# Optimization experiments

Hardware: AMD Instinct MI355X
Metric: run time of the kernel (lower is better)

## Reference

```python
import jax, jax.numpy as jnp
import numpy as np

SRC, B, SNT, E, C, V, EXT = 512, 16, 512, 512, 512, 12000, 500


def setup_inputs() -> dict:
    key = jax.random.key(0)
    ks = jax.random.split(key, 12)
    alignment_weight = jax.random.uniform(ks[0], (SRC, B, SNT), dtype=jnp.float32)
    arc_weight = jax.random.uniform(ks[1], (SRC, B, SRC), dtype=jnp.float32)
    rel_weight = jnp.zeros((1,), jnp.float32)
    concept_outs = jax.random.normal(ks[2], (SRC, B, E), dtype=jnp.float32)
    copy_seq = jax.random.randint(ks[3], (SNT, B, 2), 0, V + EXT)
    # pin the max so tot_ext = V + EXT is deterministic (torch uses copy_seq.max().item())
    copy_seq = copy_seq.at[0, 0, 0].set(V + EXT - 1)
    target = jax.random.randint(ks[4], (SRC, B), 0, V)
    target_rel = jnp.zeros((1,), jnp.int64 if jax.config.read('jax_enable_x64') else jnp.int32)
    std = 0.02
    W_transfer = jax.random.normal(ks[5], (C, E), jnp.float32) * std
    b_transfer = jnp.zeros((C,), jnp.float32)
    W_gen = jax.random.normal(ks[6], (V, C), jnp.float32) * std
    b_gen = jnp.zeros((V,), jnp.float32)
    W_div = jax.random.normal(ks[7], (3, C), jnp.float32) * std
    b_div = jnp.zeros((3,), jnp.float32)
    return dict(alignment_weight=alignment_weight, arc_weight=arc_weight,
                rel_weight=rel_weight, concept_outs=concept_outs,
                copy_seq=copy_seq, target=target, target_rel=target_rel,
                bsz=B, src_len=SRC,
                W_transfer=W_transfer, b_transfer=b_transfer,
                W_gen=W_gen, b_gen=b_gen, W_div=W_div, b_div=b_div)


def reference(alignment_weight, arc_weight, rel_weight, concept_outs, copy_seq,
              target, target_rel, bsz, src_len,
              W_transfer, b_transfer, W_gen, b_gen, W_div, b_div):
    # work=True inference path of ArcConceptDecoder (joint_rel=False, separate_rel=False)
    snt_len = alignment_weight.shape[-1]
    copy_seq = copy_seq[:snt_len]                       # [snt, B, 2]
    h = jnp.tanh(concept_outs @ W_transfer.T + b_transfer)  # [src, B, C]
    gates = jax.nn.softmax(h @ W_div.T + b_div, axis=-1)     # [src, B, 3]
    gen_gate = gates[..., 0:1]
    map_gate = gates[..., 1:2]
    copy_gate = gates[..., 2:3]
    copy_gate2 = jnp.concatenate([copy_gate, map_gate], axis=-1)  # [src, B, 2]
    probs = gen_gate * jax.nn.softmax(h @ W_gen.T + b_gen, axis=-1)  # [src, B, V]
    vocab = probs.shape[-1]
    tot_ext = vocab + EXT
    probs = jnp.concatenate(
        [probs, jnp.zeros(probs.shape[:-1] + (tot_ext - vocab,), probs.dtype)], axis=-1)
    # index: copy_seq.transpose(0,1).view(1,B,-1).expand(src,-1,-1)
    index = jnp.transpose(copy_seq, (1, 0, 2)).reshape(1, probs.shape[1], -1)  # [1, B, snt*2]
    index = jnp.broadcast_to(index, (probs.shape[0],) + index.shape[1:])       # [src, B, snt*2]
    copy_probs = (copy_gate2[:, :, None, :] * alignment_weight[..., None])
    copy_probs = copy_probs.reshape(probs.shape[0], probs.shape[1], -1)        # [src, B, snt*2]
    # scatter_add along last dim
    S, Bv = probs.shape[0], probs.shape[1]
    flat_probs = probs.reshape(S * Bv, tot_ext)
    flat_idx = index.reshape(S * Bv, -1)
    flat_cp = copy_probs.reshape(S * Bv, -1)
    rows = jnp.arange(S * Bv)[:, None]
    flat_probs = flat_probs.at[rows, flat_idx].add(flat_cp)
    probs = flat_probs.reshape(S, Bv, tot_ext)
    ll = jnp.log(probs + 1e-12)
    arc_ll = jnp.log(arc_weight + 1e-12)
    return ll, arc_ll
```

## Files before the change

kernel.cpp:

```cpp
#include <hip/hip_runtime.h>
#include <hip/hip_bf16.h>

#define SRCL 512
#define BSZ  16
#define SNTL 512
#define CDIM 512
#define KDIM 512
#define VOC  12000
#define EXTN 500
#define MROWS (SRCL*BSZ)
#define TOTV (VOC+EXTN)
#define NPAD 12032
#define LL_SIZE ((size_t)MROWS * TOTV)

typedef __attribute__((ext_vector_type(8))) short bf16x8;
typedef __attribute__((ext_vector_type(4))) float f32x4;

__device__ __forceinline__ unsigned short f2bf(float x) {
  union { __hip_bfloat16 b; unsigned short u; } c;
  c.b = __float2bfloat16(x);
  return c.u;
}
__device__ __forceinline__ float bflo(unsigned int u) { return __uint_as_float(u << 16); }
__device__ __forceinline__ float bfhi(unsigned int u) { return __uint_as_float(u & 0xffff0000u); }

__device__ __forceinline__ void gload16(const void* g, void* l) {
  __builtin_amdgcn_global_load_lds(
      (const __attribute__((address_space(1))) unsigned int*)g,
      (__attribute__((address_space(3))) unsigned int*)l, 16, 0, 0);
}

__device__ __forceinline__ float wred_max(float v) {
  for (int o = 32; o; o >>= 1) v = fmaxf(v, __shfl_down(v, o, 64));
  return v;
}
__device__ __forceinline__ float wred_sum(float v) {
  for (int o = 32; o; o >>= 1) v += __shfl_down(v, o, 64);
  return v;
}

__global__ void cvt_kernel(const float* __restrict__ co, const float* __restrict__ wt,
                           const float* __restrict__ wg,
                           unsigned short* __restrict__ cob,
                           unsigned short* __restrict__ wtb,
                           unsigned short* __restrict__ wgb) {
  const int stride = gridDim.x * blockDim.x;
  const int t0 = blockIdx.x * blockDim.x + threadIdx.x;
  for (int i = t0; i < MROWS*KDIM/4; i += stride) {
    const float4 v = ((const float4*)co)[i];
    ushort4 o; o.x = f2bf(v.x); o.y = f2bf(v.y); o.z = f2bf(v.z); o.w = f2bf(v.w);
    ((ushort4*)cob)[i] = o;
  }
  for (int i = t0; i < CDIM*KDIM/4; i += stride) {
    const float4 v = ((const float4*)wt)[i];
    ushort4 o; o.x = f2bf(v.x); o.y = f2bf(v.y); o.z = f2bf(v.z); o.w = f2bf(v.w);
    ((ushort4*)wtb)[i] = o;
  }
  for (int i = t0; i < NPAD*KDIM/4; i += stride) {
    float4 v = make_float4(0.f, 0.f, 0.f, 0.f);
    if (i < VOC*KDIM/4) v = ((const float4*)wg)[i];
    ushort4 o; o.x = f2bf(v.x); o.y = f2bf(v.y); o.z = f2bf(v.z); o.w = f2bf(v.w);
    ((ushort4*)wgb)[i] = o;
  }
}

template<int EPI>
__launch_bounds__(256)
__global__ void gemm_bt(const short* __restrict__ A, const short* __restrict__ Bm,
                        const float* __restrict__ bias, void* __restrict__ outp) {
  __shared__ short As[128*64];
  __shared__ short Bs[128*64];
  const int tid  = threadIdx.x;
  const int wave = tid >> 6;
  const int lane = tid & 63;

  const int nwg = gridDim.x * gridDim.y;
  int bid = blockIdx.y * gridDim.x + blockIdx.x;
  bid = (bid & 7) * (nwg >> 3) + (bid >> 3);
  const int bx = bid % gridDim.x;
  const int by = bid / gridDim.x;
  const int m0 = by * 128;
  const int n0 = bx * 128;

  const int srow = lane >> 3;
  const int ssk  = ((lane & 7) ^ srow) * 8;
  const size_t aBase = (size_t)(m0 + wave*32 + srow) * KDIM + ssk;
  const size_t bBase = (size_t)(n0 + wave*32 + srow) * KDIM + ssk;
  short* lA = As + wave*32*64;
  short* lB = Bs + wave*32*64;

  const int wm = wave & 1, wn = wave >> 1;
  const int quad = lane >> 4, r16 = lane & 15;
  const int rsw  = r16 & 7;
  const int aoffb = (wm*64 + r16) * 64;
  const int boffb = (wn*64 + r16) * 64;

  f32x4 acc[4][4];
#pragma unroll
  for (int i = 0; i < 4; ++i)
#pragma unroll
    for (int j = 0; j < 4; ++j) acc[i][j] = (f32x4){0.f,0.f,0.f,0.f};

  for (int kt = 0; kt < KDIM/64; ++kt) {
    const size_t ko = (size_t)kt * 64;
    __syncthreads();
#pragma unroll
    for (int j = 0; j < 4; ++j) {
      gload16(A  + aBase + ko + (size_t)j*8*KDIM, lA + j*512);
      gload16(Bm + bBase + ko + (size_t)j*8*KDIM, lB + j*512);
    }
    __syncthreads();
#pragma unroll
    for (int ks = 0; ks < 2; ++ks) {
      const int kc = ((ks*4 + quad) ^ rsw) * 8;
      bf16x8 af[4], bf[4];
#pragma unroll
      for (int i = 0; i < 4; ++i) {
        af[i] = *(const bf16x8*)(As + aoffb + i*1024 + kc);
        bf[i] = *(const bf16x8*)(Bs + boffb + i*1024 + kc);
      }
#pragma unroll
      for (int mi = 0; mi < 4; ++mi)
#pragma unroll
        for (int ni = 0; ni < 4; ++ni)
          acc[mi][ni] = __builtin_amdgcn_mfma_f32_16x16x32_bf16(af[mi], bf[ni], acc[mi][ni], 0, 0, 0);
    }
  }

#pragma unroll
  for (int mi = 0; mi < 4; ++mi) {
#pragma unroll
    for (int ni = 0; ni < 4; ++ni) {
#pragma unroll
      for (int r = 0; r < 4; ++r) {
        const int row = m0 + wm*64 + mi*16 + quad*4 + r;
        const int col = n0 + wn*64 + ni*16 + r16;
        float v = acc[mi][ni][r];
        if constexpr (EPI == 0) {
          v = tanhf(v + bias[col]);
          ((unsigned short*)outp)[(size_t)row * CDIM + col] = f2bf(v);
        } else if constexpr (EPI == 1) {
          v += (col < VOC) ? bias[col] : 0.f;
          ((float*)outp)[(size_t)row * TOTV + col] = v;
        } else {
          v += (col < VOC) ? bias[col] : 0.f;
          ((unsigned short*)outp)[(size_t)row * NPAD + col] = f2bf(v);
        }
      }
    }
  }
}

template<int BF16L>
__launch_bounds__(1024)
__global__ void finalize_kernel(const void* __restrict__ lg, float* __restrict__ out,
                                const __hip_bfloat16* __restrict__ hmat,
                                const float* __restrict__ Wd, const float* __restrict__ bd,
                                const int* __restrict__ copy_seq,
                                const float* __restrict__ align) {
  __shared__ __align__(16) float p[TOTV];
  __shared__ float scr[16];
  __shared__ float gscr[24];
  __shared__ float gv[3];
  const int m = blockIdx.x;
  const int b = m & 15;
  const int tid = threadIdx.x;
  float* row = out + (size_t)m * TOTV;

  {
    float d0 = 0.f, d1 = 0.f, d2 = 0.f;
    if (tid < CDIM) {
      const float hv = __bfloat162float(hmat[(size_t)m*CDIM + tid]);
      d0 = hv * Wd[tid];
      d1 = hv * Wd[CDIM + tid];
      d2 = hv * Wd[2*CDIM + tid];
    }
    d0 = wred_sum(d0); d1 = wred_sum(d1); d2 = wred_sum(d2);
    const int w = tid >> 6;
    if ((tid & 63) == 0 && w < 8) { gscr[w*3] = d0; gscr[w*3+1] = d1; gscr[w*3+2] = d2; }
  }
  __syncthreads();
  if (tid == 0) {
    float g0 = bd[0], g1 = bd[1], g2 = bd[2];
    for (int i = 0; i < 8; ++i) { g0 += gscr[i*3]; g1 += gscr[i*3+1]; g2 += gscr[i*3+2]; }
    const float mg = fmaxf(g0, fmaxf(g1, g2));
    const float e0 = __expf(g0-mg), e1 = __expf(g1-mg), e2 = __expf(g2-mg);
    const float inv3 = 1.f / (e0 + e1 + e2);
    gv[0] = e0*inv3; gv[1] = e1*inv3; gv[2] = e2*inv3;
  }

  float mx = -1e30f;
  if constexpr (BF16L) {
    const uint4* rowv = (const uint4*)((const unsigned short*)lg + (size_t)m * NPAD);
    for (int i = tid; i < VOC/8; i += 1024) {
      const uint4 q = rowv[i];
      float4 lo, hi;
      lo.x = bflo(q.x); lo.y = bfhi(q.x); lo.z = bflo(q.y); lo.w = bfhi(q.y);
      hi.x = bflo(q.z); hi.y = bfhi(q.z); hi.z = bflo(q.w); hi.w = bfhi(q.w);
      ((float4*)p)[i*2]   = lo;
      ((float4*)p)[i*2+1] = hi;
      mx = fmaxf(mx, fmaxf(fmaxf(fmaxf(lo.x,lo.y),fmaxf(lo.z,lo.w)),
                           fmaxf(fmaxf(hi.x,hi.y),fmaxf(hi.z,hi.w))));
    }
  } else {
    const float4* rowv = (const float4*)row;
    for (int i = tid; i < VOC/4; i += 1024) {
      const float4 v = rowv[i];
      ((float4*)p)[i] = v;
      mx = fmaxf(mx, fmaxf(fmaxf(v.x, v.y), fmaxf(v.z, v.w)));
    }
  }
  for (int i = VOC + tid; i < TOTV; i += 1024) p[i] = 0.f;

  mx = wred_max(mx);
  if ((tid & 63) == 0) scr[tid >> 6] = mx;
  __syncthreads();
  mx = scr[0];
#pragma unroll
  for (int i = 1; i < 16; ++i) mx = fmaxf(mx, scr[i]);
  __syncthreads();

  float sm = 0.f;
  for (int i = tid; i < VOC; i += 1024) {
    const float e = __expf(p[i] - mx);
    p[i] = e;
    sm += e;
  }
  sm = wred_sum(sm);
  if ((tid & 63) == 0) scr[tid >> 6] = sm;
  __syncthreads();
  sm = scr[0];
#pragma unroll
  for (int i = 1; i < 16; ++i) sm += scr[i];

  const float gen  = gv[0];
  const float mapg = gv[1];
  const float cpg  = gv[2];
  const float scale = gen / sm;
  const float inv   = sm / gen;
  const float cw = cpg * inv, mw = mapg * inv;

  if (tid < SNTL) {
    const float aw = align[(size_t)m * SNTL + tid];
    const int2 cs = *(const int2*)&copy_seq[(tid*BSZ + b)*2];
    atomicAdd(&p[cs.x], cw * aw);
    atomicAdd(&p[cs.y], mw * aw);
  }
  __syncthreads();

  for (int i = tid; i < TOTV/4; i += 1024) {
    const float4 v = ((const float4*)p)[i];
    float4 r;
    r.x = __logf(fmaf(v.x, scale, 1e-12f));
    r.y = __logf(fmaf(v.y, scale, 1e-12f));
    r.z = __logf(fmaf(v.z, scale, 1e-12f));
    r.w = __logf(fmaf(v.w, scale, 1e-12f));
    ((float4*)row)[i] = r;
  }
}

__global__ void arc_kernel(const float4* __restrict__ arc, float4* __restrict__ out) {
  const int i = blockIdx.x * blockDim.x + threadIdx.x;
  if (i < (SRCL*BSZ*SRCL)/4) {
    const float4 v = arc[i];
    float4 r;
    r.x = __logf(v.x + 1e-12f);
    r.y = __logf(v.y + 1e-12f);
    r.z = __logf(v.z + 1e-12f);
    r.w = __logf(v.w + 1e-12f);
    out[i] = r;
  }
}

extern "C" void kernel_launch(void* const* d_in, const int* in_sizes, int n_in,
                              void* d_out, int out_size, void* d_ws, size_t ws_size,
                              hipStream_t stream) {
  (void)in_sizes; (void)n_in; (void)out_size;
  const float* align   = (const float*)d_in[0];
  const float* arc     = (const float*)d_in[1];
  const float* concept = (const float*)d_in[3];
  const int*   cseq    = (const int*)d_in[4];
  const float* Wt = (const float*)d_in[9];
  const float* bt = (const float*)d_in[10];
  const float* Wg = (const float*)d_in[11];
  const float* bg = (const float*)d_in[12];
  const float* Wd = (const float*)d_in[13];
  const float* bd = (const float*)d_in[14];
  float* out = (float*)d_out;

  unsigned short* cob = (unsigned short*)d_ws;
  unsigned short* wtb = cob + (size_t)MROWS*KDIM;
  unsigned short* wgb = wtb + (size_t)CDIM*KDIM;
  unsigned short* hb  = wgb + (size_t)NPAD*KDIM;
  unsigned short* logitsb = hb + (size_t)MROWS*KDIM;
  const size_t need = (size_t)((char*)(logitsb + (size_t)MROWS*NPAD) - (char*)d_ws);
  const bool use_bf16_logits = (ws_size >= need);

  cvt_kernel<<<2048, 256, 0, stream>>>(concept, Wt, Wg, cob, wtb, wgb);
  gemm_bt<0><<<dim3(CDIM/128, MROWS/128), 256, 0, stream>>>(
      (const short*)cob, (const short*)wtb, bt, (void*)hb);
  if (use_bf16_logits) {
    gemm_bt<2><<<dim3(NPAD/128, MROWS/128), 256, 0, stream>>>(
        (const short*)hb, (const short*)wgb, bg, (void*)logitsb);
    finalize_kernel<1><<<MROWS, 1024, 0, stream>>>(
        logitsb, out, (const __hip_bfloat16*)hb, Wd, bd, cseq, align);
  } else {
    gemm_bt<1><<<dim3(NPAD/128, MROWS/128), 256, 0, stream>>>(
        (const short*)hb, (const short*)wgb, bg, (void*)out);
    finalize_kernel<0><<<MROWS, 1024, 0, stream>>>(
        out, out, (const __hip_bfloat16*)hb, Wd, bd, cseq, align);
  }
  arc_kernel<<<4096, 256, 0, stream>>>((const float4*)arc, (float4*)(out + LL_SIZE));
}
```

Before: 823.5 us.

## Add double-buffered 256x256 MFMA GEMM with staged LDS prefetch for vocab logits

Adds a new 512-thread GEMM kernel with 256x256 output tiles and two LDS buffers. It prefetches the next K-slice from global memory into LDS while MFMA work runs on the current slice, and interleaves barriers with s_setprio and sched_barrier hints so loads overlap compute. The large vocabulary projection now uses this kernel, with the aim of better data reuse and less stalling on memory. Separately, the small transfer GEMM is simplified: 32-wide K tiles, and the LDS swizzle and block remapping are removed, which may add bank conflicts and hurt cache locality there. The 128KB LDS footprint limits occupancy to one block per CU.

```diff
diff --git a/kernel.cpp b/kernel.cpp
--- a/kernel.cpp
+++ b/kernel.cpp
@@ -16,6 +16,11 @@
 typedef __attribute__((ext_vector_type(8))) short bf16x8;
 typedef __attribute__((ext_vector_type(4))) float f32x4;
 
+#define SBAR()   __builtin_amdgcn_s_barrier()
+#define SCHED0() __builtin_amdgcn_sched_barrier(0)
+#define LGKM0()  asm volatile("s_waitcnt lgkmcnt(0)" ::: "memory")
+#define VM0()    asm volatile("s_waitcnt vmcnt(0)" ::: "memory")
+
 __device__ __forceinline__ unsigned short f2bf(float x) {
   union { __hip_bfloat16 b; unsigned short u; } c;
   c.b = __float2bfloat16(x);
@@ -68,32 +73,27 @@
 __launch_bounds__(256)
 __global__ void gemm_bt(const short* __restrict__ A, const short* __restrict__ Bm,
                         const float* __restrict__ bias, void* __restrict__ outp) {
-  __shared__ short As[128*64];
-  __shared__ short Bs[128*64];
+  __shared__ short As[128*32];
+  __shared__ short Bs[128*32];
   const int tid  = threadIdx.x;
   const int wave = tid >> 6;
   const int lane = tid & 63;
-
-  const int nwg = gridDim.x * gridDim.y;
-  int bid = blockIdx.y * gridDim.x + blockIdx.x;
-  bid = (bid & 7) * (nwg >> 3) + (bid >> 3);
-  const int bx = bid % gridDim.x;
-  const int by = bid / gridDim.x;
-  const int m0 = by * 128;
-  const int n0 = bx * 128;
-
-  const int srow = lane >> 3;
-  const int ssk  = ((lane & 7) ^ srow) * 8;
-  const size_t aBase = (size_t)(m0 + wave*32 + srow) * KDIM + ssk;
-  const size_t bBase = (size_t)(n0 + wave*32 + srow) * KDIM + ssk;
-  short* lA = As + wave*32*64;
-  short* lB = Bs + wave*32*64;
+  const int m0 = blockIdx.y * 128;
+  const int n0 = blockIdx.x * 128;
+
+  const int lrow = lane >> 2;
+  const int lkof = (lane & 3) * 8;
+  const size_t aG0 = (size_t)(m0 + wave*32 + lrow) * KDIM + lkof;
+  const size_t aG1 = aG0 + (size_t)16 * KDIM;
+  const size_t bG0 = (size_t)(n0 + wave*32 + lrow) * KDIM + lkof;
+  const size_t bG1 = bG0 + (size_t)16 * KDIM;
+  short* lA0 = As + wave*1024;  short* lA1 = lA0 + 512;
+  short* lB0 = Bs + wave*1024;  short* lB1 = lB0 + 512;
 
   const int wm = wave & 1, wn = wave >> 1;
   const int quad = lane >> 4, r16 = lane & 15;
-  const int rsw  = r16 & 7;
-  const int aoffb = (wm*64 + r16) * 64;
-  const int boffb = (wn*64 + r16) * 64;
+  const int aoff = (wm*64 + r16)*32 + quad*8;
+  const int boff = (wn*64 + r16)*32 + quad*8;
 
   f32x4 acc[4][4];
 #pragma unroll
@@ -101,30 +101,25 @@
 #pragma unroll
     for (int j = 0; j < 4; ++j) acc[i][j] = (f32x4){0.f,0.f,0.f,0.f};
 
-  for (int kt = 0; kt < KDIM/64; ++kt) {
-    const size_t ko = (size_t)kt * 64;
+  for (int kt = 0; kt < KDIM/32; ++kt) {
+    const int kof = kt * 32;
     __syncthreads();
-#pragma unroll
-    for (int j = 0; j < 4; ++j) {
-      gload16(A  + aBase + ko + (size_t)j*8*KDIM, lA + j*512);
-      gload16(Bm + bBase + ko + (size_t)j*8*KDIM, lB + j*512);
-    }
+    gload16(A  + aG0 + kof, lA0);
+    gload16(A  + aG1 + kof, lA1);
+    gload16(Bm + bG0 + kof, lB0);
+    gload16(Bm + bG1 + kof, lB1);
     __syncthreads();
-#pragma unroll
-    for (int ks = 0; ks < 2; ++ks) {
-      const int kc = ((ks*4 + quad) ^ rsw) * 8;
-      bf16x8 af[4], bf[4];
-#pragma unroll
-      for (int i = 0; i < 4; ++i) {
-        af[i] = *(const bf16x8*)(As + aoffb + i*1024 + kc);
-        bf[i] = *(const bf16x8*)(Bs + boffb + i*1024 + kc);
-      }
-#pragma unroll
-      for (int mi = 0; mi < 4; ++mi)
-#pragma unroll
-        for (int ni = 0; ni < 4; ++ni)
-          acc[mi][ni] = __builtin_amdgcn_mfma_f32_16x16x32_bf16(af[mi], bf[ni], acc[mi][ni], 0, 0, 0);
-    }
+    bf16x8 af[4], bf[4];
+#pragma unroll
+    for (int i = 0; i < 4; ++i) {
+      af[i] = *(const bf16x8*)(As + aoff + i*512);
+      bf[i] = *(const bf16x8*)(Bs + boff + i*512);
+    }
+#pragma unroll
+    for (int mi = 0; mi < 4; ++mi)
+#pragma unroll
+      for (int ni = 0; ni < 4; ++ni)
+        acc[mi][ni] = __builtin_amdgcn_mfma_f32_16x16x32_bf16(af[mi], bf[ni], acc[mi][ni], 0, 0, 0);
   }
 
 #pragma unroll
@@ -151,6 +146,166 @@
   }
 }
 
+template<int EPI>
+__launch_bounds__(512, 2)
+__global__ void gemm256(const short* __restrict__ A, const short* __restrict__ Bm,
+                        const float* __restrict__ bias, void* __restrict__ outp) {
+  __shared__ short lds[2][2][256*64];
+  const int tid  = threadIdx.x;
+  const int wave = tid >> 6;
+  const int lane = tid & 63;
+  const int m0 = blockIdx.y * 256;
+  const int n0 = blockIdx.x * 256;
+
+  const int wm = wave >> 2;
+  const int wn = wave & 3;
+  const int quad = lane >> 4, r16 = lane & 15;
+
+  const int srow0 = wave*8 + (lane >> 3);
+  const int scol  = ((((lane & 7) * 16) ^ (((lane >> 5) & 1) << 5)) >> 1);
+  int goff[4];
+#pragma unroll
+  for (int h = 0; h < 2; ++h)
+#pragma unroll
+    for (int j = 0; j < 2; ++j)
+      goff[h*2+j] = (h*128 + j*64 + srow0) * KDIM + scol;
+  const short* Agp = A  + (size_t)m0 * KDIM;
+  const short* Bgp = Bm + (size_t)n0 * KDIM;
+
+  const int sx  = ((r16 >> 2) & 1) << 5;
+  const int kk0 = ((quad * 16) ^ sx) >> 1;
+  const int kk1 = ((64 + quad * 16) ^ sx) >> 1;
+  const int arow = (wm*128 + r16) * 64;
+  const int brow = (wn*64  + r16) * 64;
+
+  f32x4 acc[8][4];
+#pragma unroll
+  for (int i = 0; i < 8; ++i)
+#pragma unroll
+    for (int j = 0; j < 4; ++j) acc[i][j] = (f32x4){0.f,0.f,0.f,0.f};
+
+#pragma unroll
+  for (int h = 0; h < 2; ++h)
+#pragma unroll
+    for (int j = 0; j < 2; ++j)
+      gload16(Agp + goff[h*2+j], &lds[0][0][0] + h*8192 + j*4096 + wave*512);
+#pragma unroll
+  for (int h = 0; h < 2; ++h)
+#pragma unroll
+    for (int j = 0; j < 2; ++j)
+      gload16(Bgp + goff[h*2+j], &lds[0][1][0] + h*8192 + j*4096 + wave*512);
+  __syncthreads();
+
+  bf16x8 a0[4][2], b[4][2];
+  int cur = 0;
+#pragma unroll 2
+  for (int kt = 0; kt < KDIM/64; ++kt) {
+    const short* As_ = &lds[cur][0][0];
+    const short* Bs_ = &lds[cur][1][0];
+    short* An_ = &lds[cur^1][0][0];
+    short* Bn_ = &lds[cur^1][1][0];
+    const int kon = (kt + 1) * 64;
+    const bool pf = (kt < KDIM/64 - 1);
+
+#pragma unroll
+    for (int mi = 0; mi < 4; ++mi) {
+      a0[mi][0] = *(const bf16x8*)(As_ + arow + mi*1024 + kk0);
+      a0[mi][1] = *(const bf16x8*)(As_ + arow + mi*1024 + kk1);
+    }
+#pragma unroll
+    for (int ni = 0; ni < 2; ++ni) {
+      b[ni][0] = *(const bf16x8*)(Bs_ + brow + ni*1024 + kk0);
+      b[ni][1] = *(const bf16x8*)(Bs_ + brow + ni*1024 + kk1);
+    }
+    if (pf) {
+#pragma unroll
+      for (int h = 0; h < 2; ++h)
+#pragma unroll
+        for (int j = 0; j < 2; ++j)
+          gload16(Agp + kon + goff[h*2+j], An_ + h*8192 + j*4096 + wave*512);
+    }
+    SBAR(); LGKM0(); SCHED0();
+    __builtin_amdgcn_s_setprio(1);
+#pragma unroll
+    for (int mi = 0; mi < 4; ++mi)
+#pragma unroll
+      for (int ni = 0; ni < 2; ++ni)
+#pragma unroll
+        for (int ks = 0; ks < 2; ++ks)
+          acc[mi][ni] = __builtin_amdgcn_mfma_f32_16x16x32_bf16(a0[mi][ks], b[ni][ks], acc[mi][ni], 0, 0, 0);
+    __builtin_amdgcn_s_setprio(0); SCHED0(); SBAR();
+
+#pragma unroll
+    for (int ni = 2; ni < 4; ++ni) {
+      b[ni][0] = *(const bf16x8*)(Bs_ + brow + ni*1024 + kk0);
+      b[ni][1] = *(const bf16x8*)(Bs_ + brow + ni*1024 + kk1);
+    }
+    if (pf) {
+#pragma unroll
+      for (int h = 0; h < 2; ++h)
+#pragma unroll
+        for (int j = 0; j < 2; ++j)
+          gload16(Bgp + kon + goff[h*2+j], Bn_ + h*8192 + j*4096 + wave*512);
+    }
+    SBAR(); LGKM0(); SCHED0();
+    __builtin_amdgcn_s_setprio(1);
+#pragma unroll
+    for (int mi = 0; mi < 4; ++mi)
+#pragma unroll
+      for (int ni = 2; ni < 4; ++ni)
+#pragma unroll
+        for (int ks = 0; ks < 2; ++ks)
+          acc[mi][ni] = __builtin_amdgcn_mfma_f32_16x16x32_bf16(a0[mi][ks], b[ni][ks], acc[mi][ni], 0, 0, 0);
+    __builtin_amdgcn_s_setprio(0); SCHED0(); SBAR();
+
+#pragma unroll
+    for (int mi = 0; mi < 4; ++mi) {
+      a0[mi][0] = *(const bf16x8*)(As_ + arow + (mi+4)*1024 + kk0);
+      a0[mi][1] = *(const bf16x8*)(As_ + arow + (mi+4)*1024 + kk1);
+    }
+    SBAR(); LGKM0(); SCHED0();
+    __builtin_amdgcn_s_setprio(1);
+#pragma unroll
+    for (int mi = 0; mi < 4; ++mi)
+#pragma unroll
+      for (int ni = 2; ni < 4; ++ni)
+#pragma unroll
+        for (int ks = 0; ks < 2; ++ks)
+          acc[mi+4][ni] = __builtin_amdgcn_mfma_f32_16x16x32_bf16(a0[mi][ks], b[ni][ks], acc[mi+4][ni], 0, 0, 0);
+    __builtin_amdgcn_s_setprio(0); SCHED0(); SBAR();
+
+    __builtin_amdgcn_s_setprio(1);
+#pragma unroll
+    for (int mi = 0; mi < 4; ++mi)
+#pragma unroll
+      for (int ni = 0; ni < 2; ++ni)
+#pragma unroll
+        for (int ks = 0; ks < 2; ++ks)
+          acc[mi+4][ni] = __builtin_amdgcn_mfma_f32_16x16x32_bf16(a0[mi][ks], b[ni][ks], acc[mi+4][ni], 0, 0, 0);
+    __builtin_amdgcn_s_setprio(0); SCHED0();
+    VM0(); SCHED0(); SBAR();
+    cur ^= 1;
+  }
+
+#pragma unroll
+  for (int mi = 0; mi < 8; ++mi) {
+#pragma unroll
+    for (int ni = 0; ni < 4; ++ni) {
+#pragma unroll
+      for (int r = 0; r < 4; ++r) {
+        const int row = m0 + wm*128 + mi*16 + quad*4 + r;
+        const int col = n0 + wn*64 + ni*16 + r16;
+        float v = acc[mi][ni][r] + ((col < VOC) ? bias[col] : 0.f);
+        if constexpr (EPI == 1) {
+          ((float*)outp)[(size_t)row * TOTV + col] = v;
+        } else {
+          ((unsigned short*)outp)[(size_t)row * NPAD + col] = f2bf(v);
+        }
+      }
+    }
+  }
+}
+
 template<int BF16L>
 __launch_bounds__(1024)
 __global__ void finalize_kernel(const void* __restrict__ lg, float* __restrict__ out,
@@ -300,12 +455,12 @@
   gemm_bt<0><<<dim3(CDIM/128, MROWS/128), 256, 0, stream>>>(
       (const short*)cob, (const short*)wtb, bt, (void*)hb);
   if (use_bf16_logits) {
-    gemm_bt<2><<<dim3(NPAD/128, MROWS/128), 256, 0, stream>>>(
+    gemm256<2><<<dim3(NPAD/256, MROWS/256), 512, 0, stream>>>(
         (const short*)hb, (const short*)wgb, bg, (void*)logitsb);
     finalize_kernel<1><<<MROWS, 1024, 0, stream>>>(
         logitsb, out, (const __hip_bfloat16*)hb, Wd, bd, cseq, align);
   } else {
-    gemm_bt<1><<<dim3(NPAD/128, MROWS/128), 256, 0, stream>>>(
+    gemm256<1><<<dim3(NPAD/256, MROWS/256), 512, 0, stream>>>(
         (const short*)hb, (const short*)wgb, bg, (void*)out);
     finalize_kernel<0><<<MROWS, 1024, 0, stream>>>(
         out, out, (const __hip_bfloat16*)hb, Wd, bd, cseq, align);
```

Result: no change. 827.6 us (+0.5%).
